# Optimization experiments

Measured on AMD Instinct MI355X. Metric: run time of the kernel, lower is better.

## Reference

```python
import jax, jax.numpy as jnp
import numpy as np

N_NODES = 50000
N_EDGES = 800000
F_IN = 64
F_OUT = 64


def setup_inputs() -> dict:
    key = jax.random.key(0)
    k1, k2, k3, k4, k5 = jax.random.split(key, 5)
    x = jax.random.normal(k1, (N_NODES, F_IN), dtype=jnp.float32)
    edge_index = jax.random.randint(k2, (2, N_EDGES), 0, N_NODES, dtype=jnp.int32)
    # PyG GraphConv params: lin_rel (with bias) applied to aggregated neighbors,
    # lin_root (no bias) applied to the node's own features.
    scale = 1.0 / np.sqrt(F_IN)
    W_rel = jax.random.uniform(k3, (F_OUT, F_IN), dtype=jnp.float32, minval=-scale, maxval=scale)
    b_rel = jax.random.uniform(k4, (F_OUT,), dtype=jnp.float32, minval=-scale, maxval=scale)
    W_root = jax.random.uniform(k5, (F_OUT, F_IN), dtype=jnp.float32, minval=-scale, maxval=scale)
    return {"x": x, "W_rel": W_rel, "b_rel": b_rel, "W_root": W_root, "edge_index": edge_index}


def reference(x, W_rel, b_rel, W_root, edge_index):
    # GraphConv (aggr='add'): out = lin_rel(sum_{j in N(i)} x_j) + lin_root(x_i), then ReLU
    src, dst = edge_index[0], edge_index[1]
    # gather neighbor features along edges, scatter-add into destination nodes
    agg = jax.ops.segment_sum(x[src], dst, num_segments=x.shape[0])  # [N, F_IN]
    out = agg @ W_rel.T + b_rel + x @ W_root.T  # [N, F_OUT]
    return jax.nn.relu(out)
```

## Files before the change

### kernel.cpp

```cpp
#include <hip/hip_runtime.h>


#define FD 64
#define TN 64
#define BC 2048
#define KP 65
#define CS 16
#define TM 1024
#define GB 512

__global__ __launch_bounds__(256) void gcv5_prep(
    const float* __restrict__ W_rel, const float* __restrict__ W_root,
    float* __restrict__ WTrel, float* __restrict__ WTroot,
    int* __restrict__ tcnt, int n_cnt) {
  const int idx = blockIdx.x * 256 + threadIdx.x;
  if (idx < FD * FD) {
    const int o = idx >> 6, k = idx & 63;
    WTrel[k * FD + o] = W_rel[idx];
    WTroot[k * FD + o] = W_root[idx];
  }
  for (int i = idx; i < n_cnt; i += gridDim.x * 256) tcnt[i] = 0;
}

__global__ __launch_bounds__(256) void gcv5_bin(
    const int* __restrict__ eidx, int* __restrict__ tcnt,
    unsigned* __restrict__ tbuf, int n_edges, int n_tiles) {
  __shared__ int hcnt[TM];
  __shared__ int hbase[TM];

  const int t = threadIdx.x;
  for (int i = t; i < n_tiles; i += 256) hcnt[i] = 0;
  __syncthreads();

  const int per = (n_edges + gridDim.x - 1) / gridDim.x;
  const int e0 = blockIdx.x * per;
  const int e1 = min(e0 + per, n_edges);

  for (int e = e0 + t; e < e1; e += 256)
    atomicAdd(&hcnt[eidx[n_edges + e] >> 6], 1);
  __syncthreads();

  for (int i = t; i < n_tiles; i += 256) {
    const int c = hcnt[i];
    hbase[i] = (c > 0) ? atomicAdd(&tcnt[i * CS], c) : 0;
    hcnt[i] = 0;
  }
  __syncthreads();

  for (int e = e0 + t; e < e1; e += 256) {
    const int s = eidx[e];
    const int d = eidx[n_edges + e];
    const int tl = d >> 6;
    const int p = hbase[tl] + atomicAdd(&hcnt[tl], 1);
    if (p < BC)
      tbuf[(size_t)tl * BC + p] = ((unsigned)d << 16) | (unsigned)s;
  }
}

__global__ __launch_bounds__(512) void gcv5_main(
    const float* __restrict__ x,
    const float* __restrict__ WTrel,
    const float* __restrict__ b_rel,
    const float* __restrict__ WTroot,
    const int* __restrict__ tcnt,
    const unsigned* __restrict__ tbuf,
    float* __restrict__ out, int n_nodes) {
  __shared__ float aggT[FD * KP];
  __shared__ float xT[FD * KP];
  __shared__ unsigned short sl[BC + 64];
  __shared__ int hh[TN];
  __shared__ int oo[TN + 1];
  __shared__ int cc[TN];

  const int t = threadIdx.x;
  const int lane = t & 63;
  const int w = t >> 6;
  const int tile = blockIdx.x;
  const int node0 = tile * TN;
  const int cnt = min(tcnt[tile * CS], BC);
  const unsigned* lst = tbuf + (size_t)tile * BC;

  if (t < TN) hh[t] = 0;
  if (t < 64 && cnt + t < BC + 64) sl[cnt + t] = 0;
  {
    const int c4 = t & 15;
    const int rr = t >> 4;
#pragma unroll
    for (int p = 0; p < 2; ++p) {
      const int r = p * 32 + rr;
      const int gi = node0 + r;
      float4 v = make_float4(0.f, 0.f, 0.f, 0.f);
      if (gi < n_nodes) v = *(const float4*)(x + (size_t)gi * FD + c4 * 4);
      xT[(c4 * 4 + 0) * KP + r] = v.x;
      xT[(c4 * 4 + 1) * KP + r] = v.y;
      xT[(c4 * 4 + 2) * KP + r] = v.z;
      xT[(c4 * 4 + 3) * KP + r] = v.w;
    }
  }
  __syncthreads();

  for (int i = t; i < cnt; i += 512) atomicAdd(&hh[(lst[i] >> 16) & 63], 1);
  __syncthreads();

  if (w == 0) {
    int v = hh[lane];
    int s = v;
#pragma unroll
    for (int d = 1; d < 64; d <<= 1) {
      int u = __shfl_up(s, d, 64);
      if (lane >= d) s += u;
    }
    oo[lane] = s - v;
    cc[lane] = s - v;
    if (lane == 63) oo[64] = s;
  }
  __syncthreads();

  for (int i = t; i < cnt; i += 512) {
    const unsigned e = lst[i];
    const int d = (int)((e >> 16) & 63);
    sl[atomicAdd(&cc[d], 1)] = (unsigned short)(e & 0xFFFFu);
  }
  __syncthreads();

  const int slot = lane >> 4;
  const int fq = lane & 15;
  for (int nn = 0; nn < 8; ++nn) {
    const int d = w * 8 + nn;
    const int jb = oo[d];
    const int je = oo[d + 1];
    float4 acc = make_float4(0.f, 0.f, 0.f, 0.f);
    const int i0 = slot, i1 = 4 + slot, i2 = 8 + slot, i3 = 12 + slot;
    for (int e0 = jb; e0 < je; e0 += 16) {
      const int m = je - e0;
      const int j0 = (i0 < m) ? e0 + i0 : cnt;
      const int j1 = (i1 < m) ? e0 + i1 : cnt;
      const int j2 = (i2 < m) ? e0 + i2 : cnt;
      const int j3 = (i3 < m) ? e0 + i3 : cnt;
      const int s0 = (int)sl[j0];
      const int s1 = (int)sl[j1];
      const int s2 = (int)sl[j2];
      const int s3 = (int)sl[j3];
      const float4 f0 = *(const float4*)(x + (size_t)s0 * FD + fq * 4);
      const float4 f1 = *(const float4*)(x + (size_t)s1 * FD + fq * 4);
      const float4 f2 = *(const float4*)(x + (size_t)s2 * FD + fq * 4);
      const float4 f3 = *(const float4*)(x + (size_t)s3 * FD + fq * 4);
      acc.x += (i0 < m ? f0.x : 0.f); acc.y += (i0 < m ? f0.y : 0.f);
      acc.z += (i0 < m ? f0.z : 0.f); acc.w += (i0 < m ? f0.w : 0.f);
      acc.x += (i1 < m ? f1.x : 0.f); acc.y += (i1 < m ? f1.y : 0.f);
      acc.z += (i1 < m ? f1.z : 0.f); acc.w += (i1 < m ? f1.w : 0.f);
      acc.x += (i2 < m ? f2.x : 0.f); acc.y += (i2 < m ? f2.y : 0.f);
      acc.z += (i2 < m ? f2.z : 0.f); acc.w += (i2 < m ? f2.w : 0.f);
      acc.x += (i3 < m ? f3.x : 0.f); acc.y += (i3 < m ? f3.y : 0.f);
      acc.z += (i3 < m ? f3.z : 0.f); acc.w += (i3 < m ? f3.w : 0.f);
    }
    acc.x += __shfl_xor(acc.x, 16, 64); acc.y += __shfl_xor(acc.y, 16, 64);
    acc.z += __shfl_xor(acc.z, 16, 64); acc.w += __shfl_xor(acc.w, 16, 64);
    acc.x += __shfl_xor(acc.x, 32, 64); acc.y += __shfl_xor(acc.y, 32, 64);
    acc.z += __shfl_xor(acc.z, 32, 64); acc.w += __shfl_xor(acc.w, 32, 64);
    if (slot == 0) {
      aggT[(fq * 4 + 0) * KP + d] = acc.x;
      aggT[(fq * 4 + 1) * KP + d] = acc.y;
      aggT[(fq * 4 + 2) * KP + d] = acc.z;
      aggT[(fq * 4 + 3) * KP + d] = acc.w;
    }
  }
  __syncthreads();

  const int oq = t & 15, rq = t >> 4;
  const int o0 = oq * 4, r0 = rq * 2;
  const float4 bias = *(const float4*)(b_rel + o0);
  float acc[2][4];
#pragma unroll
  for (int ri = 0; ri < 2; ++ri) {
    acc[ri][0] = bias.x; acc[ri][1] = bias.y;
    acc[ri][2] = bias.z; acc[ri][3] = bias.w;
  }
#pragma unroll 4
  for (int k = 0; k < FD; ++k) {
    const float4 wr = *(const float4*)(WTrel + k * FD + o0);
    const float4 wo = *(const float4*)(WTroot + k * FD + o0);
    const float a0 = aggT[k * KP + r0 + 0], a1 = aggT[k * KP + r0 + 1];
    const float x0 = xT[k * KP + r0 + 0], x1 = xT[k * KP + r0 + 1];
    acc[0][0] += a0 * wr.x + x0 * wo.x; acc[0][1] += a0 * wr.y + x0 * wo.y;
    acc[0][2] += a0 * wr.z + x0 * wo.z; acc[0][3] += a0 * wr.w + x0 * wo.w;
    acc[1][0] += a1 * wr.x + x1 * wo.x; acc[1][1] += a1 * wr.y + x1 * wo.y;
    acc[1][2] += a1 * wr.z + x1 * wo.z; acc[1][3] += a1 * wr.w + x1 * wo.w;
  }
#pragma unroll
  for (int ri = 0; ri < 2; ++ri) {
    const int gi = node0 + r0 + ri;
    if (gi < n_nodes) {
      float4 o4;
      o4.x = fmaxf(acc[ri][0], 0.f); o4.y = fmaxf(acc[ri][1], 0.f);
      o4.z = fmaxf(acc[ri][2], 0.f); o4.w = fmaxf(acc[ri][3], 0.f);
      *(float4*)(out + (size_t)gi * FD + o0) = o4;
    }
  }
}

extern "C" void kernel_launch(void* const* d_in, const int* in_sizes, int n_in,
                              void* d_out, int out_size, void* d_ws, size_t ws_size,
                              hipStream_t stream) {
  const float* x      = (const float*)d_in[0];
  const float* W_rel  = (const float*)d_in[1];
  const float* b_rel  = (const float*)d_in[2];
  const float* W_root = (const float*)d_in[3];
  const int* eidx     = (const int*)d_in[4];

  const int n_nodes = in_sizes[0] / FD;
  const int n_edges = in_sizes[4] / 2;
  const int n_tiles = (n_nodes + TN - 1) / TN;

  int* tcnt      = (int*)d_ws;
  unsigned* tbuf = (unsigned*)(tcnt + (size_t)n_tiles * CS);
  float* WTrel   = (float*)(tbuf + (size_t)n_tiles * BC);
  float* WTroot  = WTrel + FD * FD;

  float* out = (float*)d_out;

  const int n_cnt = n_tiles * CS;
  const int gPrep = (n_cnt + 255) / 256;
  gcv5_prep<<<gPrep, 256, 0, stream>>>(W_rel, W_root, WTrel, WTroot, tcnt,
                                       n_cnt);

  gcv5_bin<<<GB, 256, 0, stream>>>(eidx, tcnt, tbuf, n_edges, n_tiles);

  gcv5_main<<<n_tiles, 512, 0, stream>>>(x, WTrel, b_rel, WTroot, tcnt, tbuf,
                                         out, n_nodes);
}
```

Baseline: 162.3 us.

## Halve main block size, process two nodes per wave, and halve bin grid

The main kernel now runs 256 threads per block instead of 512. Each wave handles 16 destination nodes, gathering two at a time with interleaved loads so more memory requests are in flight per wave. The epilogue GEMM computes 4 rows per thread instead of 2. The binning kernel grid also drops from 512 to 256 blocks. The aim is more memory-level parallelism per wave and lighter per-block overhead, at the cost of more registers and load imbalance when the two paired nodes have different degrees.

```diff
diff --git a/kernel.cpp b/kernel.cpp
--- a/kernel.cpp
+++ b/kernel.cpp
@@ -7,9 +7,9 @@
 #define KP 65
 #define CS 16
 #define TM 1024
-#define GB 512
-
-__global__ __launch_bounds__(256) void gcv5_prep(
+#define GB 256
+
+__global__ __launch_bounds__(256) void gcv6_prep(
     const float* __restrict__ W_rel, const float* __restrict__ W_root,
     float* __restrict__ WTrel, float* __restrict__ WTroot,
     int* __restrict__ tcnt, int n_cnt) {
@@ -22,7 +22,7 @@
   for (int i = idx; i < n_cnt; i += gridDim.x * 256) tcnt[i] = 0;
 }
 
-__global__ __launch_bounds__(256) void gcv5_bin(
+__global__ __launch_bounds__(256) void gcv6_bin(
     const int* __restrict__ eidx, int* __restrict__ tcnt,
     unsigned* __restrict__ tbuf, int n_edges, int n_tiles) {
   __shared__ int hcnt[TM];
@@ -57,7 +57,7 @@
   }
 }
 
-__global__ __launch_bounds__(512) void gcv5_main(
+__global__ __launch_bounds__(256) void gcv6_main(
     const float* __restrict__ x,
     const float* __restrict__ WTrel,
     const float* __restrict__ b_rel,
@@ -86,8 +86,8 @@
     const int c4 = t & 15;
     const int rr = t >> 4;
 #pragma unroll
-    for (int p = 0; p < 2; ++p) {
-      const int r = p * 32 + rr;
+    for (int p = 0; p < 4; ++p) {
+      const int r = p * 16 + rr;
       const int gi = node0 + r;
       float4 v = make_float4(0.f, 0.f, 0.f, 0.f);
       if (gi < n_nodes) v = *(const float4*)(x + (size_t)gi * FD + c4 * 4);
@@ -99,7 +99,7 @@
   }
   __syncthreads();
 
-  for (int i = t; i < cnt; i += 512) atomicAdd(&hh[(lst[i] >> 16) & 63], 1);
+  for (int i = t; i < cnt; i += 256) atomicAdd(&hh[(lst[i] >> 16) & 63], 1);
   __syncthreads();
 
   if (w == 0) {
@@ -116,7 +116,7 @@
   }
   __syncthreads();
 
-  for (int i = t; i < cnt; i += 512) {
+  for (int i = t; i < cnt; i += 256) {
     const unsigned e = lst[i];
     const int d = (int)((e >> 16) & 63);
     sl[atomicAdd(&cc[d], 1)] = (unsigned short)(e & 0xFFFFu);
@@ -125,54 +125,85 @@
 
   const int slot = lane >> 4;
   const int fq = lane & 15;
-  for (int nn = 0; nn < 8; ++nn) {
-    const int d = w * 8 + nn;
-    const int jb = oo[d];
-    const int je = oo[d + 1];
-    float4 acc = make_float4(0.f, 0.f, 0.f, 0.f);
-    const int i0 = slot, i1 = 4 + slot, i2 = 8 + slot, i3 = 12 + slot;
-    for (int e0 = jb; e0 < je; e0 += 16) {
-      const int m = je - e0;
-      const int j0 = (i0 < m) ? e0 + i0 : cnt;
-      const int j1 = (i1 < m) ? e0 + i1 : cnt;
-      const int j2 = (i2 < m) ? e0 + i2 : cnt;
-      const int j3 = (i3 < m) ? e0 + i3 : cnt;
-      const int s0 = (int)sl[j0];
-      const int s1 = (int)sl[j1];
-      const int s2 = (int)sl[j2];
-      const int s3 = (int)sl[j3];
-      const float4 f0 = *(const float4*)(x + (size_t)s0 * FD + fq * 4);
-      const float4 f1 = *(const float4*)(x + (size_t)s1 * FD + fq * 4);
-      const float4 f2 = *(const float4*)(x + (size_t)s2 * FD + fq * 4);
-      const float4 f3 = *(const float4*)(x + (size_t)s3 * FD + fq * 4);
-      acc.x += (i0 < m ? f0.x : 0.f); acc.y += (i0 < m ? f0.y : 0.f);
-      acc.z += (i0 < m ? f0.z : 0.f); acc.w += (i0 < m ? f0.w : 0.f);
-      acc.x += (i1 < m ? f1.x : 0.f); acc.y += (i1 < m ? f1.y : 0.f);
-      acc.z += (i1 < m ? f1.z : 0.f); acc.w += (i1 < m ? f1.w : 0.f);
-      acc.x += (i2 < m ? f2.x : 0.f); acc.y += (i2 < m ? f2.y : 0.f);
-      acc.z += (i2 < m ? f2.z : 0.f); acc.w += (i2 < m ? f2.w : 0.f);
-      acc.x += (i3 < m ? f3.x : 0.f); acc.y += (i3 < m ? f3.y : 0.f);
-      acc.z += (i3 < m ? f3.z : 0.f); acc.w += (i3 < m ? f3.w : 0.f);
-    }
-    acc.x += __shfl_xor(acc.x, 16, 64); acc.y += __shfl_xor(acc.y, 16, 64);
-    acc.z += __shfl_xor(acc.z, 16, 64); acc.w += __shfl_xor(acc.w, 16, 64);
-    acc.x += __shfl_xor(acc.x, 32, 64); acc.y += __shfl_xor(acc.y, 32, 64);
-    acc.z += __shfl_xor(acc.z, 32, 64); acc.w += __shfl_xor(acc.w, 32, 64);
+  const int i0 = slot, i1 = 4 + slot, i2 = 8 + slot, i3 = 12 + slot;
+  for (int p = 0; p < 8; ++p) {
+    const int dA = w * 16 + 2 * p;
+    const int dB = dA + 1;
+    int eA = oo[dA];
+    const int eAend = oo[dA + 1];
+    int eB = oo[dB];
+    const int eBend = oo[dB + 1];
+    float4 accA = make_float4(0.f, 0.f, 0.f, 0.f);
+    float4 accB = make_float4(0.f, 0.f, 0.f, 0.f);
+    while (eA < eAend || eB < eBend) {
+      const int mA = eAend - eA;
+      const int mB = eBend - eB;
+      const int a0 = (i0 < mA) ? eA + i0 : cnt;
+      const int a1 = (i1 < mA) ? eA + i1 : cnt;
+      const int a2 = (i2 < mA) ? eA + i2 : cnt;
+      const int a3 = (i3 < mA) ? eA + i3 : cnt;
+      const int b0 = (i0 < mB) ? eB + i0 : cnt;
+      const int b1 = (i1 < mB) ? eB + i1 : cnt;
+      const int b2 = (i2 < mB) ? eB + i2 : cnt;
+      const int b3 = (i3 < mB) ? eB + i3 : cnt;
+      const int sA0 = (int)sl[a0], sA1 = (int)sl[a1];
+      const int sA2 = (int)sl[a2], sA3 = (int)sl[a3];
+      const int sB0 = (int)sl[b0], sB1 = (int)sl[b1];
+      const int sB2 = (int)sl[b2], sB3 = (int)sl[b3];
+      const float4 fA0 = *(const float4*)(x + (size_t)sA0 * FD + fq * 4);
+      const float4 fA1 = *(const float4*)(x + (size_t)sA1 * FD + fq * 4);
+      const float4 fA2 = *(const float4*)(x + (size_t)sA2 * FD + fq * 4);
+      const float4 fA3 = *(const float4*)(x + (size_t)sA3 * FD + fq * 4);
+      const float4 fB0 = *(const float4*)(x + (size_t)sB0 * FD + fq * 4);
+      const float4 fB1 = *(const float4*)(x + (size_t)sB1 * FD + fq * 4);
+      const float4 fB2 = *(const float4*)(x + (size_t)sB2 * FD + fq * 4);
+      const float4 fB3 = *(const float4*)(x + (size_t)sB3 * FD + fq * 4);
+      accA.x += (i0 < mA ? fA0.x : 0.f); accA.y += (i0 < mA ? fA0.y : 0.f);
+      accA.z += (i0 < mA ? fA0.z : 0.f); accA.w += (i0 < mA ? fA0.w : 0.f);
+      accA.x += (i1 < mA ? fA1.x : 0.f); accA.y += (i1 < mA ? fA1.y : 0.f);
+      accA.z += (i1 < mA ? fA1.z : 0.f); accA.w += (i1 < mA ? fA1.w : 0.f);
+      accA.x += (i2 < mA ? fA2.x : 0.f); accA.y += (i2 < mA ? fA2.y : 0.f);
+      accA.z += (i2 < mA ? fA2.z : 0.f); accA.w += (i2 < mA ? fA2.w : 0.f);
+      accA.x += (i3 < mA ? fA3.x : 0.f); accA.y += (i3 < mA ? fA3.y : 0.f);
+      accA.z += (i3 < mA ? fA3.z : 0.f); accA.w += (i3 < mA ? fA3.w : 0.f);
+      accB.x += (i0 < mB ? fB0.x : 0.f); accB.y += (i0 < mB ? fB0.y : 0.f);
+      accB.z += (i0 < mB ? fB0.z : 0.f); accB.w += (i0 < mB ? fB0.w : 0.f);
+      accB.x += (i1 < mB ? fB1.x : 0.f); accB.y += (i1 < mB ? fB1.y : 0.f);
+      accB.z += (i1 < mB ? fB1.z : 0.f); accB.w += (i1 < mB ? fB1.w : 0.f);
+      accB.x += (i2 < mB ? fB2.x : 0.f); accB.y += (i2 < mB ? fB2.y : 0.f);
+      accB.z += (i2 < mB ? fB2.z : 0.f); accB.w += (i2 < mB ? fB2.w : 0.f);
+      accB.x += (i3 < mB ? fB3.x : 0.f); accB.y += (i3 < mB ? fB3.y : 0.f);
+      accB.z += (i3 < mB ? fB3.z : 0.f); accB.w += (i3 < mB ? fB3.w : 0.f);
+      eA += 16;
+      eB += 16;
+    }
+    accA.x += __shfl_xor(accA.x, 16, 64); accA.y += __shfl_xor(accA.y, 16, 64);
+    accA.z += __shfl_xor(accA.z, 16, 64); accA.w += __shfl_xor(accA.w, 16, 64);
+    accB.x += __shfl_xor(accB.x, 16, 64); accB.y += __shfl_xor(accB.y, 16, 64);
+    accB.z += __shfl_xor(accB.z, 16, 64); accB.w += __shfl_xor(accB.w, 16, 64);
+    accA.x += __shfl_xor(accA.x, 32, 64); accA.y += __shfl_xor(accA.y, 32, 64);
+    accA.z += __shfl_xor(accA.z, 32, 64); accA.w += __shfl_xor(accA.w, 32, 64);
+    accB.x += __shfl_xor(accB.x, 32, 64); accB.y += __shfl_xor(accB.y, 32, 64);
+    accB.z += __shfl_xor(accB.z, 32, 64); accB.w += __shfl_xor(accB.w, 32, 64);
     if (slot == 0) {
-      aggT[(fq * 4 + 0) * KP + d] = acc.x;
-      aggT[(fq * 4 + 1) * KP + d] = acc.y;
-      aggT[(fq * 4 + 2) * KP + d] = acc.z;
-      aggT[(fq * 4 + 3) * KP + d] = acc.w;
+      aggT[(fq * 4 + 0) * KP + dA] = accA.x;
+      aggT[(fq * 4 + 1) * KP + dA] = accA.y;
+      aggT[(fq * 4 + 2) * KP + dA] = accA.z;
+      aggT[(fq * 4 + 3) * KP + dA] = accA.w;
+      aggT[(fq * 4 + 0) * KP + dB] = accB.x;
+      aggT[(fq * 4 + 1) * KP + dB] = accB.y;
+      aggT[(fq * 4 + 2) * KP + dB] = accB.z;
+      aggT[(fq * 4 + 3) * KP + dB] = accB.w;
     }
   }
   __syncthreads();
 
   const int oq = t & 15, rq = t >> 4;
-  const int o0 = oq * 4, r0 = rq * 2;
+  const int o0 = oq * 4, r0 = rq * 4;
   const float4 bias = *(const float4*)(b_rel + o0);
-  float acc[2][4];
-#pragma unroll
-  for (int ri = 0; ri < 2; ++ri) {
+  float acc[4][4];
+#pragma unroll
+  for (int ri = 0; ri < 4; ++ri) {
     acc[ri][0] = bias.x; acc[ri][1] = bias.y;
     acc[ri][2] = bias.z; acc[ri][3] = bias.w;
   }
@@ -181,14 +212,20 @@
     const float4 wr = *(const float4*)(WTrel + k * FD + o0);
     const float4 wo = *(const float4*)(WTroot + k * FD + o0);
     const float a0 = aggT[k * KP + r0 + 0], a1 = aggT[k * KP + r0 + 1];
+    const float a2 = aggT[k * KP + r0 + 2], a3 = aggT[k * KP + r0 + 3];
     const float x0 = xT[k * KP + r0 + 0], x1 = xT[k * KP + r0 + 1];
+    const float x2 = xT[k * KP + r0 + 2], x3 = xT[k * KP + r0 + 3];
     acc[0][0] += a0 * wr.x + x0 * wo.x; acc[0][1] += a0 * wr.y + x0 * wo.y;
     acc[0][2] += a0 * wr.z + x0 * wo.z; acc[0][3] += a0 * wr.w + x0 * wo.w;
     acc[1][0] += a1 * wr.x + x1 * wo.x; acc[1][1] += a1 * wr.y + x1 * wo.y;
     acc[1][2] += a1 * wr.z + x1 * wo.z; acc[1][3] += a1 * wr.w + x1 * wo.w;
-  }
-#pragma unroll
-  for (int ri = 0; ri < 2; ++ri) {
+    acc[2][0] += a2 * wr.x + x2 * wo.x; acc[2][1] += a2 * wr.y + x2 * wo.y;
+    acc[2][2] += a2 * wr.z + x2 * wo.z; acc[2][3] += a2 * wr.w + x2 * wo.w;
+    acc[3][0] += a3 * wr.x + x3 * wo.x; acc[3][1] += a3 * wr.y + x3 * wo.y;
+    acc[3][2] += a3 * wr.z + x3 * wo.z; acc[3][3] += a3 * wr.w + x3 * wo.w;
+  }
+#pragma unroll
+  for (int ri = 0; ri < 4; ++ri) {
     const int gi = node0 + r0 + ri;
     if (gi < n_nodes) {
       float4 o4;
@@ -221,11 +258,11 @@
 
   const int n_cnt = n_tiles * CS;
   const int gPrep = (n_cnt + 255) / 256;
-  gcv5_prep<<<gPrep, 256, 0, stream>>>(W_rel, W_root, WTrel, WTroot, tcnt,
+  gcv6_prep<<<gPrep, 256, 0, stream>>>(W_rel, W_root, WTrel, WTroot, tcnt,
                                        n_cnt);
 
-  gcv5_bin<<<GB, 256, 0, stream>>>(eidx, tcnt, tbuf, n_edges, n_tiles);
-
-  gcv5_main<<<n_tiles, 512, 0, stream>>>(x, WTrel, b_rel, WTroot, tcnt, tbuf,
+  gcv6_bin<<<GB, 256, 0, stream>>>(eidx, tcnt, tbuf, n_edges, n_tiles);
+
+  gcv6_main<<<n_tiles, 256, 0, stream>>>(x, WTrel, b_rel, WTroot, tcnt, tbuf,
                                          out, n_nodes);
 }
```

After: 146.0 us. 1.11x faster.
